# Kernel optimization log

Measured on AMD Instinct MI355X. Metric: run time of the kernel, lower is better.

Reference implementation:

```python
import jax, jax.numpy as jnp
import numpy as np

N = 131072          # total sampled proposals (flattened over batch)
D = 1024            # num_extractor_out
C = 21              # num_classes (VOC: 20 + background)


def setup_inputs() -> dict:
    key = jax.random.key(0)
    k1, k2, k3 = jax.random.split(key, 3)
    features = jax.random.normal(k1, (N, D), dtype=jnp.float32)
    # Linear weights stored as [in, out] so y = x @ W + b
    W_cls = jax.random.normal(k2, (D, C), dtype=jnp.float32) * (1.0 / np.sqrt(D))
    b_cls = jnp.zeros((C,), dtype=jnp.float32)
    W_tf = jax.random.normal(k3, (D, C * 4), dtype=jnp.float32) * (1.0 / np.sqrt(D))
    b_tf = jnp.zeros((C * 4,), dtype=jnp.float32)
    return {"features": features, "W_cls": W_cls, "b_cls": b_cls, "W_tf": W_tf, "b_tf": b_tf}


def reference(features, W_cls, b_cls, W_tf, b_tf):
    # ROI.forward with identity extractor / no pre/post transforms.
    proposal_classes = features @ W_cls + b_cls                    # [N, C]
    proposal_transformers = features @ W_tf + b_tf                 # [N, C*4]
    proposal_transformers = proposal_transformers.reshape(features.shape[0], C, 4)
    return proposal_classes, proposal_transformers
```

## Files before the change

kernel.cpp:

```cpp
#include <hip/hip_runtime.h>
#include <hip/hip_bf16.h>

#define NROWS 131072
#define DK    1024
#define CCLS  21
#define CTF   84
#define NCOL  105
#define NKT   (DK/32)
#define NCT   7
#define BM    128

typedef __attribute__((ext_vector_type(4))) float f32x4;
typedef __attribute__((ext_vector_type(8))) short bf16x8;

__device__ __forceinline__ unsigned short f2bf_rne(float x) {
    union { float f; unsigned u; } v; v.f = x;
    unsigned r = v.u + 0x7fffu + ((v.u >> 16) & 1u);
    return (unsigned short)(r >> 16);
}

__device__ __forceinline__ unsigned pack2(float lo, float hi) {
    union { float f; unsigned u; } a, b; a.f = lo; b.f = hi;
    return ((a.u + 0x8000u) >> 16) | ((b.u + 0x8000u) & 0xffff0000u);
}

__device__ __forceinline__ bf16x8 cvt8(const f32x4 lo, const f32x4 hi) {
    union { unsigned u[4]; bf16x8 v; } r;
    r.u[0] = pack2(lo[0], lo[1]);
    r.u[1] = pack2(lo[2], lo[3]);
    r.u[2] = pack2(hi[0], hi[1]);
    r.u[3] = pack2(hi[2], hi[3]);
    return r.v;
}

__global__ void pack_B_kernel(const float* __restrict__ Wc,
                              const float* __restrict__ Wt,
                              unsigned short* __restrict__ Bp) {
    const int frag = blockIdx.x;
    const int kt = frag / NCT, ct = frag % NCT;
    const int lane = threadIdx.x;
    const int col = ct * 16 + (lane & 15);
    const int k0  = kt * 32 + ((lane >> 4) << 3);
    bf16x8 o;
#pragma unroll
    for (int j = 0; j < 8; ++j) {
        const int k = k0 + j;
        float v = 0.0f;
        if (col < CCLS)      v = Wc[k * CCLS + col];
        else if (col < NCOL) v = Wt[k * CTF + (col - CCLS)];
        o[j] = (short)f2bf_rne(v);
    }
    *reinterpret_cast<bf16x8*>(Bp + ((size_t)frag * 64 + lane) * 8) = o;
}

__global__ __launch_bounds__(256, 4)
void roi_gemm_kernel(const float* __restrict__ F,
                     const unsigned short* __restrict__ Bp,
                     const float* __restrict__ bcls,
                     const float* __restrict__ btf,
                     float* __restrict__ out) {
    const int t    = threadIdx.x;
    const int wave = t >> 6;
    const int lane = t & 63;
    const int fr   = lane & 15;
    const int fk   = (lane >> 4) * 8;

    const long rw = (long)blockIdx.x * BM + wave * 32;
    const float* pa0 = F + (size_t)(rw + fr) * DK + fk;
    const float* pa1 = pa0 + (size_t)16 * DK;

    f32x4 acc[2][NCT];
#pragma unroll
    for (int a = 0; a < 2; ++a)
#pragma unroll
        for (int b = 0; b < NCT; ++b)
            acc[a][b] = (f32x4){0.f, 0.f, 0.f, 0.f};

    const unsigned short* bb = Bp + (size_t)lane * 8;

    for (int kt = 0; kt < NKT; ++kt) {
        const f32x4 a0lo = *reinterpret_cast<const f32x4*>(pa0 + kt * 32);
        const f32x4 a0hi = *reinterpret_cast<const f32x4*>(pa0 + kt * 32 + 4);
        const f32x4 a1lo = *reinterpret_cast<const f32x4*>(pa1 + kt * 32);
        const f32x4 a1hi = *reinterpret_cast<const f32x4*>(pa1 + kt * 32 + 4);

        bf16x8 bfrag[NCT];
#pragma unroll
        for (int ct = 0; ct < NCT; ++ct)
            bfrag[ct] = *reinterpret_cast<const bf16x8*>(
                bb + ((size_t)kt * NCT + ct) * 64 * 8);

        const bf16x8 af0 = cvt8(a0lo, a0hi);
        const bf16x8 af1 = cvt8(a1lo, a1hi);

#pragma unroll
        for (int ct = 0; ct < NCT; ++ct) {
            acc[0][ct] = __builtin_amdgcn_mfma_f32_16x16x32_bf16(
                af0, bfrag[ct], acc[0][ct], 0, 0, 0);
            acc[1][ct] = __builtin_amdgcn_mfma_f32_16x16x32_bf16(
                af1, bfrag[ct], acc[1][ct], 0, 0, 0);
        }
    }

    float* out_tf = out + (size_t)NROWS * CCLS;
#pragma unroll
    for (int rt = 0; rt < 2; ++rt) {
        const long rbase = rw + rt * 16 + ((lane >> 4) << 2);
#pragma unroll
        for (int ct = 0; ct < NCT; ++ct) {
            const int col = ct * 16 + fr;
            if (col >= NCOL) continue;
            const float bias = (col < CCLS) ? bcls[col] : btf[col - CCLS];
#pragma unroll
            for (int j = 0; j < 4; ++j) {
                const long row = rbase + j;
                const float v = acc[rt][ct][j] + bias;
                if (col < CCLS) out[row * CCLS + col] = v;
                else            out_tf[row * CTF + (col - CCLS)] = v;
            }
        }
    }
}

extern "C" void kernel_launch(void* const* d_in, const int* in_sizes, int n_in,
                              void* d_out, int out_size, void* d_ws, size_t ws_size,
                              hipStream_t stream) {
    const float* F  = (const float*)d_in[0];
    const float* Wc = (const float*)d_in[1];
    const float* bc = (const float*)d_in[2];
    const float* Wt = (const float*)d_in[3];
    const float* bt = (const float*)d_in[4];
    unsigned short* Bp = (unsigned short*)d_ws;

    pack_B_kernel<<<NKT * NCT, 64, 0, stream>>>(Wc, Wt, Bp);
    roi_gemm_kernel<<<NROWS / BM, 256, 0, stream>>>(F, Bp, bc, bt, (float*)d_out);
}
```

Baseline: 172.1 us.

## Stage 16-row A tiles in LDS with split-K across waves and reduce

Each block now handles 16 rows, strided across the matrix (row = r*8192 + block). It loads them with fully coalesced float4 reads, converts them to bf16 and stores them into a swizzled LDS tile. Each wave computes a quarter of K with MFMA, and the partial accumulators are reduced through LDS before the biased outputs are written. The aim is to replace the strided per-lane global A loads with coalesced streaming and to raise block count and parallelism. In exchange it adds LDS traffic, two extra barriers, and scattered output writes caused by the strided row mapping.

```diff
diff --git a/kernel.cpp b/kernel.cpp
--- a/kernel.cpp
+++ b/kernel.cpp
@@ -6,12 +6,12 @@
 #define CCLS  21
 #define CTF   84
 #define NCOL  105
-#define NKT   (DK/32)
 #define NCT   7
-#define BM    128
+#define NBLK  8192
 
 typedef __attribute__((ext_vector_type(4))) float f32x4;
 typedef __attribute__((ext_vector_type(8))) short bf16x8;
+typedef __attribute__((ext_vector_type(2))) unsigned int u32x2;
 
 __device__ __forceinline__ unsigned short f2bf_rne(float x) {
     union { float f; unsigned u; } v; v.f = x;
@@ -22,15 +22,6 @@
 __device__ __forceinline__ unsigned pack2(float lo, float hi) {
     union { float f; unsigned u; } a, b; a.f = lo; b.f = hi;
     return ((a.u + 0x8000u) >> 16) | ((b.u + 0x8000u) & 0xffff0000u);
-}
-
-__device__ __forceinline__ bf16x8 cvt8(const f32x4 lo, const f32x4 hi) {
-    union { unsigned u[4]; bf16x8 v; } r;
-    r.u[0] = pack2(lo[0], lo[1]);
-    r.u[1] = pack2(lo[2], lo[3]);
-    r.u[2] = pack2(hi[0], hi[1]);
-    r.u[3] = pack2(hi[2], hi[3]);
-    return r.v;
 }
 
 __global__ void pack_B_kernel(const float* __restrict__ Wc,
@@ -53,72 +44,92 @@
     *reinterpret_cast<bf16x8*>(Bp + ((size_t)frag * 64 + lane) * 8) = o;
 }
 
-__global__ __launch_bounds__(256, 4)
+__global__ __launch_bounds__(256)
 void roi_gemm_kernel(const float* __restrict__ F,
                      const unsigned short* __restrict__ Bp,
                      const float* __restrict__ bcls,
                      const float* __restrict__ btf,
                      float* __restrict__ out) {
+    __shared__ __align__(16) unsigned char smem[16 * 2048];
+
     const int t    = threadIdx.x;
     const int wave = t >> 6;
     const int lane = t & 63;
     const int fr   = lane & 15;
-    const int fk   = (lane >> 4) * 8;
+    const int fq   = lane >> 4;
+    const int b    = blockIdx.x;
 
-    const long rw = (long)blockIdx.x * BM + wave * 32;
-    const float* pa0 = F + (size_t)(rw + fr) * DK + fk;
-    const float* pa1 = pa0 + (size_t)16 * DK;
+    const int rcol0 = (t >> 2) & 15;
+    float biasr[NCT];
+#pragma unroll
+    for (int ct = 0; ct < NCT; ++ct) {
+        const int col = ct * 16 + rcol0;
+        biasr[ct] = (col < CCLS) ? bcls[col]
+                  : (col < NCOL) ? btf[col - CCLS] : 0.0f;
+    }
 
-    f32x4 acc[2][NCT];
 #pragma unroll
-    for (int a = 0; a < 2; ++a)
+    for (int half = 0; half < 2; ++half) {
+        f32x4 v[8];
 #pragma unroll
-        for (int b = 0; b < NCT; ++b)
-            acc[a][b] = (f32x4){0.f, 0.f, 0.f, 0.f};
+        for (int j = 0; j < 8; ++j)
+            v[j] = *reinterpret_cast<const f32x4*>(
+                F + ((size_t)(half * 8 + j) * NBLK + b) * DK + t * 4);
+#pragma unroll
+        for (int j = 0; j < 8; ++j) {
+            const int R = half * 8 + j;
+            u32x2 d;
+            d[0] = pack2(v[j][0], v[j][1]);
+            d[1] = pack2(v[j][2], v[j][3]);
+            *reinterpret_cast<u32x2*>(
+                smem + R * 2048 + (((t >> 1) ^ (R & 7)) << 4) + ((t & 1) << 3)) = d;
+        }
+    }
+    __syncthreads();
+
+    f32x4 acc[NCT];
+#pragma unroll
+    for (int ct = 0; ct < NCT; ++ct) acc[ct] = (f32x4){0.f, 0.f, 0.f, 0.f};
 
     const unsigned short* bb = Bp + (size_t)lane * 8;
+    const int w8 = wave * 8;
 
-    for (int kt = 0; kt < NKT; ++kt) {
-        const f32x4 a0lo = *reinterpret_cast<const f32x4*>(pa0 + kt * 32);
-        const f32x4 a0hi = *reinterpret_cast<const f32x4*>(pa0 + kt * 32 + 4);
-        const f32x4 a1lo = *reinterpret_cast<const f32x4*>(pa1 + kt * 32);
-        const f32x4 a1hi = *reinterpret_cast<const f32x4*>(pa1 + kt * 32 + 4);
-
-        bf16x8 bfrag[NCT];
+#pragma unroll
+    for (int jj = 0; jj < 8; ++jj) {
+        const int kt = w8 + jj;
+        bf16x8 bfr[NCT];
 #pragma unroll
         for (int ct = 0; ct < NCT; ++ct)
-            bfrag[ct] = *reinterpret_cast<const bf16x8*>(
-                bb + ((size_t)kt * NCT + ct) * 64 * 8);
-
-        const bf16x8 af0 = cvt8(a0lo, a0hi);
-        const bf16x8 af1 = cvt8(a1lo, a1hi);
-
+            bfr[ct] = *reinterpret_cast<const bf16x8*>(
+                bb + ((size_t)(kt * NCT + ct) * 512));
+        const bf16x8 a = *reinterpret_cast<const bf16x8*>(
+            smem + fr * 2048 + ((((kt << 2) | fq) ^ (fr & 7)) << 4));
 #pragma unroll
-        for (int ct = 0; ct < NCT; ++ct) {
-            acc[0][ct] = __builtin_amdgcn_mfma_f32_16x16x32_bf16(
-                af0, bfrag[ct], acc[0][ct], 0, 0, 0);
-            acc[1][ct] = __builtin_amdgcn_mfma_f32_16x16x32_bf16(
-                af1, bfrag[ct], acc[1][ct], 0, 0, 0);
-        }
+        for (int ct = 0; ct < NCT; ++ct)
+            acc[ct] = __builtin_amdgcn_mfma_f32_16x16x32_bf16(
+                a, bfr[ct], acc[ct], 0, 0, 0);
     }
 
+    __syncthreads();
+#pragma unroll
+    for (int ct = 0; ct < NCT; ++ct)
+        *reinterpret_cast<f32x4*>(
+            smem + (((wave * NCT + ct) << 10) + (lane << 4))) = acc[ct];
+    __syncthreads();
+
+    const float* sf = reinterpret_cast<const float*>(smem);
     float* out_tf = out + (size_t)NROWS * CCLS;
+    const long grow = (long)(((t >> 6) << 2) + (t & 3)) * NBLK + b;
 #pragma unroll
-    for (int rt = 0; rt < 2; ++rt) {
-        const long rbase = rw + rt * 16 + ((lane >> 4) << 2);
-#pragma unroll
-        for (int ct = 0; ct < NCT; ++ct) {
-            const int col = ct * 16 + fr;
-            if (col >= NCOL) continue;
-            const float bias = (col < CCLS) ? bcls[col] : btf[col - CCLS];
-#pragma unroll
-            for (int j = 0; j < 4; ++j) {
-                const long row = rbase + j;
-                const float v = acc[rt][ct][j] + bias;
-                if (col < CCLS) out[row * CCLS + col] = v;
-                else            out_tf[row * CTF + (col - CCLS)] = v;
-            }
-        }
+    for (int ct = 0; ct < NCT; ++ct) {
+        const int col = ct * 16 + rcol0;
+        if (col >= NCOL) continue;
+        const float v = sf[(0 * NCT + ct) * 256 + t] +
+                        sf[(1 * NCT + ct) * 256 + t] +
+                        sf[(2 * NCT + ct) * 256 + t] +
+                        sf[(3 * NCT + ct) * 256 + t] + biasr[ct];
+        if (col < CCLS) out[grow * CCLS + col] = v;
+        else            out_tf[grow * CTF + (col - CCLS)] = v;
     }
 }
 
@@ -132,6 +143,6 @@
     const float* bt = (const float*)d_in[4];
     unsigned short* Bp = (unsigned short*)d_ws;
 
-    pack_B_kernel<<<NKT * NCT, 64, 0, stream>>>(Wc, Wt, Bp);
-    roi_gemm_kernel<<<NROWS / BM, 256, 0, stream>>>(F, Bp, bc, bt, (float*)d_out);
+    pack_B_kernel<<<NCT * (DK / 32), 64, 0, stream>>>(Wc, Wt, Bp);
+    roi_gemm_kernel<<<NBLK, 256, 0, stream>>>(F, Bp, bc, bt, (float*)d_out);
 }
```

Result: no change. 174.8 us (+1.6%).
